# Performance work log

Hardware: AMD Instinct MI355X
Metric: run time of the kernel (lower is better)

Reference implementation:

```python
import jax, jax.numpy as jnp
import numpy as np

N_EMBD = 64
HEAD_SIZE = 64
BLOCK_SIZE = 256


def setup_inputs() -> dict:
    key = jax.random.key(0)
    ks = jax.random.split(key, 7)
    B, T = 1024, 256
    inputs = jax.random.normal(ks[0], (B, T, N_EMBD), dtype=jnp.float32)
    s = 1.0 / np.sqrt(N_EMBD)
    Wq = jax.random.uniform(ks[1], (HEAD_SIZE, N_EMBD), jnp.float32, -s, s)
    Wk = jax.random.uniform(ks[2], (HEAD_SIZE, N_EMBD), jnp.float32, -s, s)
    Wv = jax.random.uniform(ks[3], (HEAD_SIZE, N_EMBD), jnp.float32, -s, s)
    bq = jax.random.uniform(ks[4], (HEAD_SIZE,), jnp.float32, -s, s)
    bk = jax.random.uniform(ks[5], (HEAD_SIZE,), jnp.float32, -s, s)
    bv = jax.random.uniform(ks[6], (HEAD_SIZE,), jnp.float32, -s, s)
    return {"inputs": inputs, "Wq": Wq, "bq": bq, "Wk": Wk, "bk": bk, "Wv": Wv, "bv": bv}


def reference(inputs, Wq, bq, Wk, bk, Wv, bv):
    # inputs: [B, T, C]; Linear weights stored torch-style [out, in]
    T = inputs.shape[1]
    Q = jnp.einsum('btc,hc->bth', inputs, Wq) + bq  # [B,T,H]
    K = jnp.einsum('btc,hc->bth', inputs, Wk) + bk
    V = jnp.einsum('btc,hc->bth', inputs, Wv) + bv
    scale = 1.0 / jnp.sqrt(jnp.float32(K.shape[-1]))
    scores = jnp.einsum('bth,bsh->bts', Q, K) * scale  # [B,T,T]
    causal = jnp.triu(jnp.ones((T, T), dtype=bool), k=1)
    scores = jnp.where(causal, jnp.float32(-1e9), scores)
    attn = jax.nn.softmax(scores, axis=-1)
    return jnp.einsum('bts,bsh->bth', attn, V)
```

## Files before the change

### kernel.cpp

```cpp
#include <hip/hip_runtime.h>

typedef __attribute__((ext_vector_type(8))) __bf16 bf16x8;
typedef __attribute__((ext_vector_type(4))) float f32x4;
typedef __attribute__((ext_vector_type(4))) unsigned int u32x4;
typedef __attribute__((ext_vector_type(2))) unsigned int u32x2;

#define LDS_SCR 0
#define LDS_K   10240
#define LDS_VT  43008
#define LDS_TOT 75776
#define W_Q (LDS_VT)
#define W_K (LDS_VT + 8192)
#define W_V (LDS_VT + 16384)

static __device__ __forceinline__ unsigned int cvt_pk_bf16(float a, float b) {
  unsigned int r;
  asm("v_cvt_pk_bf16_f32 %0, %1, %2" : "=v"(r) : "v"(a), "v"(b));
  return r;
}
static __device__ __forceinline__ int swz128(int row, int colbyte) {
  return row * 128 + (colbyte ^ ((row & 7) << 4));
}
static __device__ __forceinline__ int swz512(int row, int colbyte) {
  return row * 512 + (colbyte ^ ((row & 7) << 4));
}
static __device__ __forceinline__ bf16x8 ldx(const float* p) {
  const float4* p4 = (const float4*)p;
  float4 lo = p4[0], hi = p4[1];
  u32x4 u;
  u.x = cvt_pk_bf16(lo.x, lo.y); u.y = cvt_pk_bf16(lo.z, lo.w);
  u.z = cvt_pk_bf16(hi.x, hi.y); u.w = cvt_pk_bf16(hi.z, hi.w);
  return __builtin_bit_cast(bf16x8, u);
}

__global__ __launch_bounds__(512, 4)
void head_fused(const float* __restrict__ x,
                const float* __restrict__ Wq, const float* __restrict__ bq,
                const float* __restrict__ Wk, const float* __restrict__ bk,
                const float* __restrict__ Wv, const float* __restrict__ bv,
                float* __restrict__ out)
{
  __shared__ __align__(16) char smem[LDS_TOT];
  const int b    = blockIdx.x;
  const int tid  = threadIdx.x;
  const int lane = tid & 63;
  const int wid  = tid >> 6;
  const int g    = lane >> 4;
  const int ln   = lane & 15;
  const int tA   = wid;
  const int tB   = 15 - wid;

  const float* xb = x + (size_t)b * (256 * 64);
  char* scr = smem + LDS_SCR + wid * 1280;

  bf16x8 xfA[2], xfB[2];
#pragma unroll
  for (int ks = 0; ks < 2; ++ks) {
    xfA[ks] = ldx(xb + (tA * 16 + ln) * 64 + ks * 32 + g * 8);
    xfB[ks] = ldx(xb + (tB * 16 + ln) * 64 + ks * 32 + g * 8);
  }

#pragma unroll
  for (int i = 0; i < 6; ++i) {
    int idx = tid + i * 512;
    int mat = idx >> 10;
    int rem = idx & 1023;
    const float4* wg = (const float4*)(mat == 0 ? Wq : (mat == 1 ? Wk : Wv));
    float4 v = wg[rem];
    int e = rem * 4;
    int h = e >> 6, c = e & 63;
    u32x2 p;
    p.x = cvt_pk_bf16(v.x, v.y);
    p.y = cvt_pk_bf16(v.z, v.w);
    *(u32x2*)(smem + W_Q + mat * 8192 + swz128(h, c * 2)) = p;
  }
  __syncthreads();

  bf16x8 qaA[2], qaB[2];
#pragma unroll
  for (int ti = 0; ti < 2; ++ti) {
    bf16x8 xf0 = ti ? xfB[0] : xfA[0];
    bf16x8 xf1 = ti ? xfB[1] : xfA[1];
#pragma unroll
    for (int hk = 0; hk < 2; ++hk) {
#pragma unroll
      for (int mt2 = 0; mt2 < 2; ++mt2) {
        int mt = hk * 2 + mt2;
        float4 bb = *(const float4*)(bq + mt * 16 + g * 4);
        f32x4 acc = {0.f, 0.f, 0.f, 0.f};
        {
          u32x4 u = *(const u32x4*)(smem + W_Q + swz128(mt * 16 + ln, (0 * 32 + g * 8) * 2));
          acc = __builtin_amdgcn_mfma_f32_16x16x32_bf16(__builtin_bit_cast(bf16x8, u), xf0, acc, 0, 0, 0);
        }
        {
          u32x4 u = *(const u32x4*)(smem + W_Q + swz128(mt * 16 + ln, (1 * 32 + g * 8) * 2));
          acc = __builtin_amdgcn_mfma_f32_16x16x32_bf16(__builtin_bit_cast(bf16x8, u), xf1, acc, 0, 0, 0);
        }
        u32x2 p;
        p.x = cvt_pk_bf16((acc[0] + bb.x) * 0.125f, (acc[1] + bb.y) * 0.125f);
        p.y = cvt_pk_bf16((acc[2] + bb.z) * 0.125f, (acc[3] + bb.w) * 0.125f);
        *(u32x2*)(scr + ln * 80 + mt2 * 32 + g * 8) = p;
      }
      u32x4 u = *(const u32x4*)(scr + ln * 80 + g * 16);
      if (ti) qaB[hk] = __builtin_bit_cast(bf16x8, u);
      else    qaA[hk] = __builtin_bit_cast(bf16x8, u);
    }
  }

#pragma unroll
  for (int ti = 0; ti < 2; ++ti) {
    int tile = ti ? tB : tA;
    bf16x8 xf0 = ti ? xfB[0] : xfA[0];
    bf16x8 xf1 = ti ? xfB[1] : xfA[1];
#pragma unroll
    for (int mt = 0; mt < 4; ++mt) {
      float4 bb = *(const float4*)(bk + mt * 16 + g * 4);
      f32x4 acc = {0.f, 0.f, 0.f, 0.f};
      {
        u32x4 u = *(const u32x4*)(smem + W_K + swz128(mt * 16 + ln, (0 * 32 + g * 8) * 2));
        acc = __builtin_amdgcn_mfma_f32_16x16x32_bf16(__builtin_bit_cast(bf16x8, u), xf0, acc, 0, 0, 0);
      }
      {
        u32x4 u = *(const u32x4*)(smem + W_K + swz128(mt * 16 + ln, (1 * 32 + g * 8) * 2));
        acc = __builtin_amdgcn_mfma_f32_16x16x32_bf16(__builtin_bit_cast(bf16x8, u), xf1, acc, 0, 0, 0);
      }
      u32x2 p;
      p.x = cvt_pk_bf16(acc[0] + bb.x, acc[1] + bb.y);
      p.y = cvt_pk_bf16(acc[2] + bb.z, acc[3] + bb.w);
      *(u32x2*)(smem + LDS_K + swz128(tile * 16 + ln, (mt * 16 + g * 4) * 2)) = p;
    }
  }

  bf16x8 wv[4][2];
  float bvv[4];
#pragma unroll
  for (int nf = 0; nf < 4; ++nf) {
    bvv[nf] = bv[nf * 16 + ln];
#pragma unroll
    for (int ks = 0; ks < 2; ++ks) {
      u32x4 u = *(const u32x4*)(smem + W_V + swz128(nf * 16 + ln, (ks * 32 + g * 8) * 2));
      wv[nf][ks] = __builtin_bit_cast(bf16x8, u);
    }
  }
  __syncthreads();

#pragma unroll
  for (int ti = 0; ti < 2; ++ti) {
    int tile = ti ? tB : tA;
    bf16x8 xf0 = ti ? xfB[0] : xfA[0];
    bf16x8 xf1 = ti ? xfB[1] : xfA[1];
#pragma unroll
    for (int nf = 0; nf < 4; ++nf) {
      f32x4 acc = {0.f, 0.f, 0.f, 0.f};
      acc = __builtin_amdgcn_mfma_f32_16x16x32_bf16(xf0, wv[nf][0], acc, 0, 0, 0);
      acc = __builtin_amdgcn_mfma_f32_16x16x32_bf16(xf1, wv[nf][1], acc, 0, 0, 0);
      int t0 = tile * 16 + g * 4;
      u32x2 p;
      p.x = cvt_pk_bf16(acc[0] + bvv[nf], acc[1] + bvv[nf]);
      p.y = cvt_pk_bf16(acc[2] + bvv[nf], acc[3] + bvv[nf]);
      *(u32x2*)(smem + LDS_VT + swz512(nf * 16 + ln, t0 * 2)) = p;
    }
  }
  __syncthreads();

  float* og = out + (size_t)b * (256 * 64);
#pragma unroll
  for (int ti = 0; ti < 2; ++ti) {
    const int tile = ti ? tB : tA;
    bf16x8 qa0 = ti ? qaB[0] : qaA[0];
    bf16x8 qa1 = ti ? qaB[1] : qaA[1];
    const int qbase = tile * 16;
    const int jmaxT = qbase >> 6;

    float mrun = -1e30f, lrun = 0.f;
    f32x4 oacc[4];
#pragma unroll
    for (int nf = 0; nf < 4; ++nf)
      oacc[nf] = (f32x4){0.f, 0.f, 0.f, 0.f};

    for (int jt = 0; jt <= jmaxT; ++jt) {
      f32x4 s[4];
#pragma unroll
      for (int nk = 0; nk < 4; ++nk)
        s[nk] = (f32x4){0.f, 0.f, 0.f, 0.f};
#pragma unroll
      for (int ks = 0; ks < 2; ++ks) {
        bf16x8 qk = ks ? qa1 : qa0;
        bf16x8 kb[4];
#pragma unroll
        for (int nk = 0; nk < 4; ++nk) {
          int key = jt * 64 + nk * 16 + ln;
          u32x4 u = *(const u32x4*)(smem + LDS_K + swz128(key, (ks * 32 + g * 8) * 2));
          kb[nk] = __builtin_bit_cast(bf16x8, u);
        }
#pragma unroll
        for (int nk = 0; nk < 4; ++nk)
          s[nk] = __builtin_amdgcn_mfma_f32_16x16x32_bf16(kb[nk], qk, s[nk], 0, 0, 0);
      }
      if (jt == jmaxT) {
        int q_abs = qbase + ln;
#pragma unroll
        for (int nk = 0; nk < 4; ++nk) {
          int keybase = jt * 64 + nk * 16 + g * 4;
#pragma unroll
          for (int d = 0; d < 4; ++d)
            s[nk][d] = (keybase + d > q_abs) ? -1e30f : s[nk][d];
        }
      }
      {
        f32x4 m4;
#pragma unroll
        for (int d = 0; d < 4; ++d)
          m4[d] = fmaxf(fmaxf(s[0][d], s[1][d]), fmaxf(s[2][d], s[3][d]));
        float mx = fmaxf(fmaxf(m4[0], m4[1]), fmaxf(m4[2], m4[3]));
        mx = fmaxf(mx, __shfl_xor(mx, 16));
        mx = fmaxf(mx, __shfl_xor(mx, 32));
        float mn = fmaxf(mrun, mx);
        float a  = __expf(mrun - mn);
        mrun = mn;
        float sum = 0.f;
#pragma unroll
        for (int nk = 0; nk < 4; ++nk)
#pragma unroll
          for (int d = 0; d < 4; ++d) {
            float p = __expf(s[nk][d] - mn);
            s[nk][d] = p;
            sum += p;
          }
        sum += __shfl_xor(sum, 16);
        sum += __shfl_xor(sum, 32);
        lrun = lrun * a + sum;
#pragma unroll
        for (int d = 0; d < 4; ++d) {
          float ad = __shfl(a, g * 4 + d);
#pragma unroll
          for (int nf = 0; nf < 4; ++nf)
            oacc[nf][d] *= ad;
        }
      }
#pragma unroll
      for (int h2 = 0; h2 < 2; ++h2) {
#pragma unroll
        for (int n2 = 0; n2 < 2; ++n2) {
          f32x4 sv = s[h2 * 2 + n2];
          u32x2 p;
          p.x = cvt_pk_bf16(sv[0], sv[1]);
          p.y = cvt_pk_bf16(sv[2], sv[3]);
          *(u32x2*)(scr + ln * 80 + n2 * 32 + g * 8) = p;
        }
        bf16x8 pa;
        {
          u32x4 u = *(const u32x4*)(scr + ln * 80 + g * 16);
          pa = __builtin_bit_cast(bf16x8, u);
        }
        bf16x8 vb[4];
#pragma unroll
        for (int nf = 0; nf < 4; ++nf) {
          int key0 = jt * 64 + h2 * 32 + g * 8;
          u32x4 u = *(const u32x4*)(smem + LDS_VT + swz512(nf * 16 + ln, key0 * 2));
          vb[nf] = __builtin_bit_cast(bf16x8, u);
        }
#pragma unroll
        for (int nf = 0; nf < 4; ++nf)
          oacc[nf] = __builtin_amdgcn_mfma_f32_16x16x32_bf16(pa, vb[nf], oacc[nf], 0, 0, 0);
      }
    }

    {
      float linv = 1.0f / lrun;
      float inv[4];
#pragma unroll
      for (int d = 0; d < 4; ++d) inv[d] = __shfl(linv, g * 4 + d);
#pragma unroll
      for (int nf = 0; nf < 4; ++nf)
#pragma unroll
        for (int d = 0; d < 4; ++d) {
          int t = qbase + g * 4 + d;
          og[t * 64 + nf * 16 + ln] = oacc[nf][d] * inv[d];
        }
    }
  }
}

extern "C" void kernel_launch(void* const* d_in, const int* in_sizes, int n_in,
                              void* d_out, int out_size, void* d_ws, size_t ws_size,
                              hipStream_t stream) {
  (void)in_sizes; (void)n_in; (void)d_ws; (void)ws_size; (void)out_size;
  const float* x  = (const float*)d_in[0];
  const float* Wq = (const float*)d_in[1];
  const float* bq = (const float*)d_in[2];
  const float* Wk = (const float*)d_in[3];
  const float* bk = (const float*)d_in[4];
  const float* Wv = (const float*)d_in[5];
  const float* bv = (const float*)d_in[6];
  float* out = (float*)d_out;
  hipLaunchKernelGGL(head_fused, dim3(1024), dim3(512), 0, stream,
                     x, Wq, bq, Wk, bk, Wv, bv, out);
}
```

Measured before the change: 41.17 us.

## Software-pipeline attention loop with fully unrolled, interleaved QK and PV stages

Splits the attention loop body into QK, mask, softmax, PV and epilogue helpers. It replaces the runtime loop over key tiles with fully unrolled straight-line schedules specialised by warp group (wid<4 vs wid>=4). The QK product for the next key tile is issued before the softmax/PV of the current one, using two score buffers, so MFMA latency and LDS reads can overlap with the exp/shuffle work. It also drops the runtime loop and mask branches, at the cost of more register pressure and a hardcoded tile-count schedule that only holds for T=256.

```diff
diff --git a/kernel.cpp b/kernel.cpp
--- a/kernel.cpp
+++ b/kernel.cpp
@@ -31,6 +31,114 @@
   u.x = cvt_pk_bf16(lo.x, lo.y); u.y = cvt_pk_bf16(lo.z, lo.w);
   u.z = cvt_pk_bf16(hi.x, hi.y); u.w = cvt_pk_bf16(hi.z, hi.w);
   return __builtin_bit_cast(bf16x8, u);
+}
+
+static __device__ __forceinline__ void qk_unit(const char* smemK, int ln, int g,
+    bf16x8 q0, bf16x8 q1, int jt, f32x4 (&s)[4])
+{
+#pragma unroll
+  for (int nk = 0; nk < 4; ++nk) s[nk] = (f32x4){0.f, 0.f, 0.f, 0.f};
+#pragma unroll
+  for (int ks = 0; ks < 2; ++ks) {
+    bf16x8 qk = ks ? q1 : q0;
+    bf16x8 kb[4];
+#pragma unroll
+    for (int nk = 0; nk < 4; ++nk) {
+      u32x4 u = *(const u32x4*)(smemK + swz128(jt * 64 + nk * 16 + ln, (ks * 32 + g * 8) * 2));
+      kb[nk] = __builtin_bit_cast(bf16x8, u);
+    }
+#pragma unroll
+    for (int nk = 0; nk < 4; ++nk)
+      s[nk] = __builtin_amdgcn_mfma_f32_16x16x32_bf16(kb[nk], qk, s[nk], 0, 0, 0);
+  }
+}
+static __device__ __forceinline__ void mask_unit(f32x4 (&s)[4], int jt, int q_abs, int g)
+{
+#pragma unroll
+  for (int nk = 0; nk < 4; ++nk) {
+    int keybase = jt * 64 + nk * 16 + g * 4;
+#pragma unroll
+    for (int d = 0; d < 4; ++d)
+      s[nk][d] = (keybase + d > q_abs) ? -1e30f : s[nk][d];
+  }
+}
+static __device__ __forceinline__ void smax_unit(f32x4 (&s)[4], float& mrun, float& lrun,
+                                                 f32x4 (&oacc)[4], int g)
+{
+  f32x4 m4;
+#pragma unroll
+  for (int d = 0; d < 4; ++d)
+    m4[d] = fmaxf(fmaxf(s[0][d], s[1][d]), fmaxf(s[2][d], s[3][d]));
+  float mx = fmaxf(fmaxf(m4[0], m4[1]), fmaxf(m4[2], m4[3]));
+  mx = fmaxf(mx, __shfl_xor(mx, 16));
+  mx = fmaxf(mx, __shfl_xor(mx, 32));
+  float mn = fmaxf(mrun, mx);
+  float a  = __expf(mrun - mn);
+  mrun = mn;
+  float sum = 0.f;
+#pragma unroll
+  for (int nk = 0; nk < 4; ++nk)
+#pragma unroll
+    for (int d = 0; d < 4; ++d) {
+      float p = __expf(s[nk][d] - mn);
+      s[nk][d] = p;
+      sum += p;
+    }
+  sum += __shfl_xor(sum, 16);
+  sum += __shfl_xor(sum, 32);
+  lrun = lrun * a + sum;
+#pragma unroll
+  for (int d = 0; d < 4; ++d) {
+    float ad = __shfl(a, g * 4 + d);
+#pragma unroll
+    for (int nf = 0; nf < 4; ++nf)
+      oacc[nf][d] *= ad;
+  }
+}
+static __device__ __forceinline__ void pv_unit(char* scr, const char* smemVT, int ln, int g,
+                                               int jt, f32x4 (&s)[4], f32x4 (&oacc)[4])
+{
+#pragma unroll
+  for (int h2 = 0; h2 < 2; ++h2) {
+#pragma unroll
+    for (int n2 = 0; n2 < 2; ++n2) {
+      f32x4 sv = s[h2 * 2 + n2];
+      u32x2 p;
+      p.x = cvt_pk_bf16(sv[0], sv[1]);
+      p.y = cvt_pk_bf16(sv[2], sv[3]);
+      *(u32x2*)(scr + ln * 80 + n2 * 32 + g * 8) = p;
+    }
+    bf16x8 pa;
+    {
+      u32x4 u = *(const u32x4*)(scr + ln * 80 + g * 16);
+      pa = __builtin_bit_cast(bf16x8, u);
+    }
+    bf16x8 vb[4];
+#pragma unroll
+    for (int nf = 0; nf < 4; ++nf) {
+      int key0 = jt * 64 + h2 * 32 + g * 8;
+      u32x4 u = *(const u32x4*)(smemVT + swz512(nf * 16 + ln, key0 * 2));
+      vb[nf] = __builtin_bit_cast(bf16x8, u);
+    }
+#pragma unroll
+    for (int nf = 0; nf < 4; ++nf)
+      oacc[nf] = __builtin_amdgcn_mfma_f32_16x16x32_bf16(pa, vb[nf], oacc[nf], 0, 0, 0);
+  }
+}
+static __device__ __forceinline__ void epi_unit(float* og, f32x4 (&oacc)[4], float lrun,
+                                                int qbase, int ln, int g)
+{
+  float linv = 1.0f / lrun;
+  float inv[4];
+#pragma unroll
+  for (int d = 0; d < 4; ++d) inv[d] = __shfl(linv, g * 4 + d);
+#pragma unroll
+  for (int nf = 0; nf < 4; ++nf)
+#pragma unroll
+    for (int d = 0; d < 4; ++d) {
+      int t = qbase + g * 4 + d;
+      og[t * 64 + nf * 16 + ln] = oacc[nf][d] * inv[d];
+    }
 }
 
 __global__ __launch_bounds__(512, 4)
@@ -164,121 +272,59 @@
   __syncthreads();
 
   float* og = out + (size_t)b * (256 * 64);
-#pragma unroll
-  for (int ti = 0; ti < 2; ++ti) {
-    const int tile = ti ? tB : tA;
-    bf16x8 qa0 = ti ? qaB[0] : qaA[0];
-    bf16x8 qa1 = ti ? qaB[1] : qaA[1];
-    const int qbase = tile * 16;
-    const int jmaxT = qbase >> 6;
-
-    float mrun = -1e30f, lrun = 0.f;
-    f32x4 oacc[4];
-#pragma unroll
-    for (int nf = 0; nf < 4; ++nf)
-      oacc[nf] = (f32x4){0.f, 0.f, 0.f, 0.f};
-
-    for (int jt = 0; jt <= jmaxT; ++jt) {
-      f32x4 s[4];
-#pragma unroll
-      for (int nk = 0; nk < 4; ++nk)
-        s[nk] = (f32x4){0.f, 0.f, 0.f, 0.f};
-#pragma unroll
-      for (int ks = 0; ks < 2; ++ks) {
-        bf16x8 qk = ks ? qa1 : qa0;
-        bf16x8 kb[4];
-#pragma unroll
-        for (int nk = 0; nk < 4; ++nk) {
-          int key = jt * 64 + nk * 16 + ln;
-          u32x4 u = *(const u32x4*)(smem + LDS_K + swz128(key, (ks * 32 + g * 8) * 2));
-          kb[nk] = __builtin_bit_cast(bf16x8, u);
-        }
-#pragma unroll
-        for (int nk = 0; nk < 4; ++nk)
-          s[nk] = __builtin_amdgcn_mfma_f32_16x16x32_bf16(kb[nk], qk, s[nk], 0, 0, 0);
-      }
-      if (jt == jmaxT) {
-        int q_abs = qbase + ln;
-#pragma unroll
-        for (int nk = 0; nk < 4; ++nk) {
-          int keybase = jt * 64 + nk * 16 + g * 4;
-#pragma unroll
-          for (int d = 0; d < 4; ++d)
-            s[nk][d] = (keybase + d > q_abs) ? -1e30f : s[nk][d];
-        }
-      }
-      {
-        f32x4 m4;
-#pragma unroll
-        for (int d = 0; d < 4; ++d)
-          m4[d] = fmaxf(fmaxf(s[0][d], s[1][d]), fmaxf(s[2][d], s[3][d]));
-        float mx = fmaxf(fmaxf(m4[0], m4[1]), fmaxf(m4[2], m4[3]));
-        mx = fmaxf(mx, __shfl_xor(mx, 16));
-        mx = fmaxf(mx, __shfl_xor(mx, 32));
-        float mn = fmaxf(mrun, mx);
-        float a  = __expf(mrun - mn);
-        mrun = mn;
-        float sum = 0.f;
-#pragma unroll
-        for (int nk = 0; nk < 4; ++nk)
-#pragma unroll
-          for (int d = 0; d < 4; ++d) {
-            float p = __expf(s[nk][d] - mn);
-            s[nk][d] = p;
-            sum += p;
-          }
-        sum += __shfl_xor(sum, 16);
-        sum += __shfl_xor(sum, 32);
-        lrun = lrun * a + sum;
-#pragma unroll
-        for (int d = 0; d < 4; ++d) {
-          float ad = __shfl(a, g * 4 + d);
-#pragma unroll
-          for (int nf = 0; nf < 4; ++nf)
-            oacc[nf][d] *= ad;
-        }
-      }
-#pragma unroll
-      for (int h2 = 0; h2 < 2; ++h2) {
-#pragma unroll
-        for (int n2 = 0; n2 < 2; ++n2) {
-          f32x4 sv = s[h2 * 2 + n2];
-          u32x2 p;
-          p.x = cvt_pk_bf16(sv[0], sv[1]);
-          p.y = cvt_pk_bf16(sv[2], sv[3]);
-          *(u32x2*)(scr + ln * 80 + n2 * 32 + g * 8) = p;
-        }
-        bf16x8 pa;
-        {
-          u32x4 u = *(const u32x4*)(scr + ln * 80 + g * 16);
-          pa = __builtin_bit_cast(bf16x8, u);
-        }
-        bf16x8 vb[4];
-#pragma unroll
-        for (int nf = 0; nf < 4; ++nf) {
-          int key0 = jt * 64 + h2 * 32 + g * 8;
-          u32x4 u = *(const u32x4*)(smem + LDS_VT + swz512(nf * 16 + ln, key0 * 2));
-          vb[nf] = __builtin_bit_cast(bf16x8, u);
-        }
-#pragma unroll
-        for (int nf = 0; nf < 4; ++nf)
-          oacc[nf] = __builtin_amdgcn_mfma_f32_16x16x32_bf16(pa, vb[nf], oacc[nf], 0, 0, 0);
-      }
-    }
-
-    {
-      float linv = 1.0f / lrun;
-      float inv[4];
-#pragma unroll
-      for (int d = 0; d < 4; ++d) inv[d] = __shfl(linv, g * 4 + d);
-#pragma unroll
-      for (int nf = 0; nf < 4; ++nf)
-#pragma unroll
-        for (int d = 0; d < 4; ++d) {
-          int t = qbase + g * 4 + d;
-          og[t * 64 + nf * 16 + ln] = oacc[nf][d] * inv[d];
-        }
-    }
+  const char* smemK  = smem + LDS_K;
+  const char* smemVT = smem + LDS_VT;
+  const int qA = tA * 16, qB = tB * 16;
+
+  float mA = -1e30f, lA = 0.f, mB = -1e30f, lB = 0.f;
+  f32x4 oA[4], oB[4];
+#pragma unroll
+  for (int nf = 0; nf < 4; ++nf) {
+    oA[nf] = (f32x4){0.f, 0.f, 0.f, 0.f};
+    oB[nf] = (f32x4){0.f, 0.f, 0.f, 0.f};
+  }
+  f32x4 s0[4], s1[4];
+
+  if (wid < 4) {
+    qk_unit(smemK, ln, g, qaA[0], qaA[1], 0, s0);
+    qk_unit(smemK, ln, g, qaB[0], qaB[1], 0, s1);
+    mask_unit(s0, 0, qA + ln, g);
+    smax_unit(s0, mA, lA, oA, g);
+    pv_unit(scr, smemVT, ln, g, 0, s0, oA);
+    epi_unit(og, oA, lA, qA, ln, g);
+    qk_unit(smemK, ln, g, qaB[0], qaB[1], 1, s0);
+    smax_unit(s1, mB, lB, oB, g);
+    pv_unit(scr, smemVT, ln, g, 0, s1, oB);
+    qk_unit(smemK, ln, g, qaB[0], qaB[1], 2, s1);
+    smax_unit(s0, mB, lB, oB, g);
+    pv_unit(scr, smemVT, ln, g, 1, s0, oB);
+    qk_unit(smemK, ln, g, qaB[0], qaB[1], 3, s0);
+    smax_unit(s1, mB, lB, oB, g);
+    pv_unit(scr, smemVT, ln, g, 2, s1, oB);
+    mask_unit(s0, 3, qB + ln, g);
+    smax_unit(s0, mB, lB, oB, g);
+    pv_unit(scr, smemVT, ln, g, 3, s0, oB);
+    epi_unit(og, oB, lB, qB, ln, g);
+  } else {
+    qk_unit(smemK, ln, g, qaA[0], qaA[1], 0, s0);
+    qk_unit(smemK, ln, g, qaA[0], qaA[1], 1, s1);
+    smax_unit(s0, mA, lA, oA, g);
+    pv_unit(scr, smemVT, ln, g, 0, s0, oA);
+    qk_unit(smemK, ln, g, qaB[0], qaB[1], 0, s0);
+    mask_unit(s1, 1, qA + ln, g);
+    smax_unit(s1, mA, lA, oA, g);
+    pv_unit(scr, smemVT, ln, g, 1, s1, oA);
+    epi_unit(og, oA, lA, qA, ln, g);
+    qk_unit(smemK, ln, g, qaB[0], qaB[1], 1, s1);
+    smax_unit(s0, mB, lB, oB, g);
+    pv_unit(scr, smemVT, ln, g, 0, s0, oB);
+    qk_unit(smemK, ln, g, qaB[0], qaB[1], 2, s0);
+    smax_unit(s1, mB, lB, oB, g);
+    pv_unit(scr, smemVT, ln, g, 1, s1, oB);
+    mask_unit(s0, 2, qB + ln, g);
+    smax_unit(s0, mB, lB, oB, g);
+    pv_unit(scr, smemVT, ln, g, 2, s0, oB);
+    epi_unit(og, oB, lB, qB, ln, g);
   }
 }
 
```

Measured after the change: 51.85 us. 26.0% more time.
